# Optimization experiments

Hardware: AMD Instinct MI355X
Metric: run time of the kernel (lower is better)

Reference implementation:

```python
import jax, jax.numpy as jnp
import numpy as np

B, T, D = 2, 1024, 1024
NUM_HEADS_ARG = 16
HS = D // NUM_HEADS_ARG          # 64 (per-head size)
H = HS                           # bug in source: num_heads passed = head_size -> 64 heads
FF = 4 * D
EPS = 1e-5


def _layernorm(x, gamma, beta):
    mu = jnp.mean(x, axis=-1, keepdims=True)
    var = jnp.mean(jnp.square(x - mu), axis=-1, keepdims=True)
    return (x - mu) * jax.lax.rsqrt(var + EPS) * gamma + beta


def setup_inputs() -> dict:
    key = jax.random.key(0)
    ks = jax.random.split(key, 12)
    s_d = 1.0 / np.sqrt(D)
    s_cat = 1.0 / np.sqrt(H * HS)
    s_ff = 1.0 / np.sqrt(FF)
    return {
        "x": jax.random.normal(ks[0], (B, T, D), jnp.float32),
        "Wq": jax.random.uniform(ks[1], (H, D, HS), jnp.float32, -s_d, s_d),
        "Wk": jax.random.uniform(ks[2], (H, D, HS), jnp.float32, -s_d, s_d),
        "Wv": jax.random.uniform(ks[3], (H, D, HS), jnp.float32, -s_d, s_d),
        "Wo": jax.random.uniform(ks[4], (H * HS, D), jnp.float32, -s_cat, s_cat),
        "bo": jax.random.uniform(ks[5], (D,), jnp.float32, -s_cat, s_cat),
        "W1": jax.random.uniform(ks[6], (D, FF), jnp.float32, -s_d, s_d),
        "b1": jax.random.uniform(ks[7], (FF,), jnp.float32, -s_d, s_d),
        "W2": jax.random.uniform(ks[8], (FF, D), jnp.float32, -s_ff, s_ff),
        "b2": jax.random.uniform(ks[9], (D,), jnp.float32, -s_ff, s_ff),
        "g1": jnp.ones((D,), jnp.float32),
        "be1": jnp.zeros((D,), jnp.float32),
        "g2": jnp.ones((D,), jnp.float32),
        "be2": jnp.zeros((D,), jnp.float32),
    }


def reference(x, Wq, Wk, Wv, Wo, bo, W1, b1, W2, b2, g1, be1, g2, be2):
    # per-head projections (no bias): [B,H,T,hs]
    q = jnp.einsum('btd,hde->bhte', x, Wq)
    k = jnp.einsum('btd,hde->bhte', x, Wk)
    v = jnp.einsum('btd,hde->bhte', x, Wv)
    scores = jnp.einsum('bhte,bhse->bhts', q, k) / np.sqrt(HS)  # [B,H,T,T]
    causal = jnp.tril(jnp.ones((T, T), bool))
    scores = jnp.where(causal, scores, -jnp.inf)
    probs = jax.nn.softmax(scores, axis=-1)
    att = jnp.einsum('bhts,bhse->bhte', probs, v)               # [B,H,T,hs]
    # torch stack(dim=3) -> [B,T,hs,H] then flatten: index = d*H + h
    cat = jnp.transpose(att, (0, 2, 3, 1)).reshape(B, T, HS * H)
    mha = cat @ Wo + bo
    x1 = _layernorm(x + mha, g1, be1)
    ff = jax.nn.relu(x1 @ W1 + b1) @ W2 + b2
    return _layernorm(x1 + ff, g2, be2)
```

## Files before the change

### kernel.cpp

```cpp
#include <hip/hip_runtime.h>

typedef unsigned short u16;
typedef __bf16 bf16x8 __attribute__((ext_vector_type(8)));
typedef float f32x4 __attribute__((ext_vector_type(4)));

#define B_ 2
#define T_ 1024
#define D_ 1024
#define H_ 64
#define HS_ 64
#define FF_ 4096
#define SZ_QKV 8388608L
#define S_SCALE 0.1803368801111f

__device__ __forceinline__ float bf2f(u16 u) {
  union { unsigned int v; float f; } x; x.v = ((unsigned int)u) << 16; return x.f;
}
__device__ __forceinline__ u16 f2bf(float f) {
  union { float f; unsigned int v; } x; x.f = f;
  unsigned int r = x.v + 0x7fffu + ((x.v >> 16) & 1u);
  return (u16)(r >> 16);
}
__device__ __forceinline__ u16 f2bf_rtz(float f) {
  union { float f; unsigned int v; } x; x.f = f;
  return (u16)(x.v >> 16);
}

typedef __attribute__((address_space(3))) unsigned int lds_u32;
typedef __attribute__((address_space(1))) const unsigned int glb_u32;
__device__ __forceinline__ void gload_lds16(const void* g, void* l) {
  __builtin_amdgcn_global_load_lds((glb_u32*)g, (lds_u32*)l, 16, 0, 0);
}

__global__ __launch_bounds__(256) void prep(
    const float* __restrict__ x, const float* __restrict__ Wq,
    const float* __restrict__ Wk, const float* __restrict__ Wv,
    const float* __restrict__ Wo, const float* __restrict__ W1,
    const float* __restrict__ W2,
    u16* __restrict__ xb, u16* __restrict__ Wqkvt, u16* __restrict__ Wot,
    u16* __restrict__ W1t, u16* __restrict__ W2t)
{
  __shared__ float tile[64][65];
  int id = blockIdx.x;
  if (id < 1024) {
    const long i = ((long)id * 256 + threadIdx.x) * 8;
    float4 a = *(const float4*)(x + i);
    float4 b = *(const float4*)(x + i + 4);
    union { uint4 v; u16 u[8]; } o;
    o.u[0]=f2bf(a.x); o.u[1]=f2bf(a.y); o.u[2]=f2bf(a.z); o.u[3]=f2bf(a.w);
    o.u[4]=f2bf(b.x); o.u[5]=f2bf(b.y); o.u[6]=f2bf(b.z); o.u[7]=f2bf(b.w);
    *(uint4*)(xb + i) = o.v;
    return;
  }
  id -= 1024;
  const float* in; u16* out; long ibase, obase; int in_rs, out_rs, r0, c0;
  if (id < 3072) {
    const int w = id >> 10, rem = id & 1023;
    const int z = rem >> 4, rt = rem & 15;
    in = (w == 0) ? Wq : (w == 1) ? Wk : Wv;
    ibase = (long)z * 65536; in_rs = 64; r0 = rt * 64; c0 = 0;
    out = Wqkvt + (long)w * 4194304;
    obase = (long)z * 65536; out_rs = 1024;
  } else if (id < 4096) {
    const int rem = id - 3072;
    const int z = rem >> 4, ct = rem & 15;
    in = Wo; ibase = (long)z * 1024; in_rs = 65536; r0 = 0; c0 = ct * 64;
    out = Wot; obase = (long)z * 64; out_rs = 4096;
  } else if (id < 5120) {
    const int rem = id - 4096;
    const int rt = rem >> 6, ct = rem & 63;
    in = W1; ibase = 0; in_rs = 4096; r0 = rt * 64; c0 = ct * 64;
    out = W1t; obase = 0; out_rs = 1024;
  } else {
    const int rem = id - 5120;
    const int rt = rem >> 4, ct = rem & 15;
    in = W2; ibase = 0; in_rs = 1024; r0 = rt * 64; c0 = ct * 64;
    out = W2t; obase = 0; out_rs = 4096;
  }
  const int t = threadIdx.x, lr = t >> 4, lc4 = (t & 15) * 4;
  #pragma unroll
  for (int j = 0; j < 4; ++j) {
    float4 f = *(const float4*)(in + ibase + (long)(r0 + lr + j * 16) * in_rs + c0 + lc4);
    tile[lr + j * 16][lc4]     = f.x;
    tile[lr + j * 16][lc4 + 1] = f.y;
    tile[lr + j * 16][lc4 + 2] = f.z;
    tile[lr + j * 16][lc4 + 3] = f.w;
  }
  __syncthreads();
  const int cr = t >> 3, ch = t & 7;
  #pragma unroll
  for (int j2 = 0; j2 < 2; ++j2) {
    const int crr = cr + j2 * 32;
    union { uint4 v; u16 u[8]; } o;
    #pragma unroll
    for (int i = 0; i < 8; ++i) o.u[i] = f2bf(tile[ch * 8 + i][crr]);
    *(uint4*)(out + obase + (long)(c0 + crr) * out_rs + r0 + ch * 8) = o.v;
  }
}

template<int EPI, int LDA, int LDB>
__global__ __launch_bounds__(512, 2) void gemm8b(
    const u16* __restrict__ A, const u16* __restrict__ Bt, u16* __restrict__ C,
    const float* __restrict__ bias, int K, int koff, int ldc)
{
  __shared__ __attribute__((aligned(16))) u16 As[3][256 * 64];
  __shared__ __attribute__((aligned(16))) u16 Bs[3][128 * 64];
  const int nwg = gridDim.x, cpx = nwg >> 3;
  const int sid = (blockIdx.x & 7) * cpx + (blockIdx.x >> 3);
  const int bm = sid & 7, bn = sid >> 3;
  const int bz = blockIdx.z;
  const long ko = (long)bz * koff;
  const int tid = threadIdx.x, wave = tid >> 6, lane = tid & 63;
  const int quad = lane >> 4, l16 = lane & 15;
  const int wm = (wave >> 1) * 64;
  const int wn = (wave & 1) * 64;
  const int slog = ((tid & 7) ^ ((tid >> 3) & 7)) * 8;
  const int srow = tid >> 3;
  const int ph0 = ((quad)     ^ (l16 & 7)) * 8;
  const int ph1 = ((4 + quad) ^ (l16 & 7)) * 8;

  const u16* Ag = A + (long)(bm * 256) * LDA + ko + slog;
  const u16* Bg = Bt + (long)(bn * 128) * LDB + ko + slog;

  f32x4 acc[4][4];
  #pragma unroll
  for (int i = 0; i < 4; ++i)
    #pragma unroll
    for (int j = 0; j < 4; ++j) acc[i][j] = (f32x4){0.f, 0.f, 0.f, 0.f};

  const int nK = K >> 6;

  auto STAGE_A = [&](int d, int t, int a) {
    gload_lds16(Ag + (long)(a * 64 + srow) * LDA + (t << 6),
                (u16*)As[d] + a * 4096 + tid * 8);
  };
  auto STAGE_B = [&](int d, int t, int b) {
    gload_lds16(Bg + (long)(b * 64 + srow) * LDB + (t << 6),
                (u16*)Bs[d] + b * 4096 + tid * 8);
  };

  #pragma unroll
  for (int a = 0; a < 4; ++a) STAGE_A(0, 0, a);
  STAGE_B(0, 0, 0); STAGE_B(0, 0, 1);
  #pragma unroll
  for (int a = 0; a < 4; ++a) STAGE_A(1, 1, a);
  STAGE_B(1, 1, 0); STAGE_B(1, 1, 1);

  bf16x8 af[4][2], bf[4][2];
  int cur = 0;
  for (int t = 0; t < nK; ++t) {
    const int nxt = (cur >= 1) ? cur - 1 : 2;
    const bool st = (t + 2) < nK;
    const u16* Ab = As[cur];
    const u16* Bb = Bs[cur];

    if (t < nK - 1) { asm volatile("s_waitcnt vmcnt(6)" ::: "memory"); }
    else            { asm volatile("s_waitcnt vmcnt(0)" ::: "memory"); }
    __builtin_amdgcn_sched_barrier(0);
    __builtin_amdgcn_s_barrier();
    __builtin_amdgcn_sched_barrier(0);

    #pragma unroll
    for (int ii = 0; ii < 2; ++ii) {
      const u16* r = Ab + (wm + ii * 16 + l16) * 64;
      af[ii][0] = *(const bf16x8*)(r + ph0);
      af[ii][1] = *(const bf16x8*)(r + ph1);
    }
    #pragma unroll
    for (int jj = 0; jj < 2; ++jj) {
      const u16* r = Bb + (wn + jj * 16 + l16) * 64;
      bf[jj][0] = *(const bf16x8*)(r + ph0);
      bf[jj][1] = *(const bf16x8*)(r + ph1);
    }
    if (st) { STAGE_A(nxt, t + 2, 0); STAGE_A(nxt, t + 2, 1); }
    __builtin_amdgcn_sched_barrier(0);
    __builtin_amdgcn_s_setprio(1);
    #pragma unroll
    for (int ks = 0; ks < 2; ++ks)
      #pragma unroll
      for (int ii = 0; ii < 2; ++ii)
        #pragma unroll
        for (int jj = 0; jj < 2; ++jj)
          acc[ii][jj] = __builtin_amdgcn_mfma_f32_16x16x32_bf16(af[ii][ks], bf[jj][ks], acc[ii][jj], 0, 0, 0);
    __builtin_amdgcn_s_setprio(0);
    __builtin_amdgcn_sched_barrier(0);

    #pragma unroll
    for (int jj = 0; jj < 2; ++jj) {
      const u16* r = Bb + (wn + (2 + jj) * 16 + l16) * 64;
      bf[2 + jj][0] = *(const bf16x8*)(r + ph0);
      bf[2 + jj][1] = *(const bf16x8*)(r + ph1);
    }
    if (st) { STAGE_A(nxt, t + 2, 2); STAGE_A(nxt, t + 2, 3); }
    __builtin_amdgcn_sched_barrier(0);
    __builtin_amdgcn_s_setprio(1);
    #pragma unroll
    for (int ks = 0; ks < 2; ++ks)
      #pragma unroll
      for (int ii = 0; ii < 2; ++ii)
        #pragma unroll
        for (int jj = 0; jj < 2; ++jj)
          acc[ii][2 + jj] = __builtin_amdgcn_mfma_f32_16x16x32_bf16(af[ii][ks], bf[2 + jj][ks], acc[ii][2 + jj], 0, 0, 0);
    __builtin_amdgcn_s_setprio(0);
    __builtin_amdgcn_sched_barrier(0);

    #pragma unroll
    for (int ii = 0; ii < 2; ++ii) {
      const u16* r = Ab + (wm + (2 + ii) * 16 + l16) * 64;
      af[2 + ii][0] = *(const bf16x8*)(r + ph0);
      af[2 + ii][1] = *(const bf16x8*)(r + ph1);
    }
    if (st) { STAGE_B(nxt, t + 2, 0); STAGE_B(nxt, t + 2, 1); }
    __builtin_amdgcn_sched_barrier(0);
    __builtin_amdgcn_s_setprio(1);
    #pragma unroll
    for (int ks = 0; ks < 2; ++ks)
      #pragma unroll
      for (int ii = 0; ii < 2; ++ii)
        #pragma unroll
        for (int jj = 0; jj < 2; ++jj)
          acc[2 + ii][jj] = __builtin_amdgcn_mfma_f32_16x16x32_bf16(af[2 + ii][ks], bf[jj][ks], acc[2 + ii][jj], 0, 0, 0);
    __builtin_amdgcn_s_setprio(0);
    __builtin_amdgcn_sched_barrier(0);

    __builtin_amdgcn_s_setprio(1);
    #pragma unroll
    for (int ks = 0; ks < 2; ++ks)
      #pragma unroll
      for (int ii = 0; ii < 2; ++ii)
        #pragma unroll
        for (int jj = 0; jj < 2; ++jj)
          acc[2 + ii][2 + jj] = __builtin_amdgcn_mfma_f32_16x16x32_bf16(af[2 + ii][ks], bf[2 + jj][ks], acc[2 + ii][2 + jj], 0, 0, 0);
    __builtin_amdgcn_s_setprio(0);

    cur = (cur == 2) ? 0 : cur + 1;
  }

  float bv[4];
  #pragma unroll
  for (int j = 0; j < 4; ++j)
    bv[j] = (EPI == 1) ? bias[bn * 128 + wn + j * 16 + l16] : 0.f;
  #pragma unroll
  for (int i = 0; i < 4; ++i) {
    #pragma unroll
    for (int r = 0; r < 4; ++r) {
      const int row = bm * 256 + wm + i * 16 + quad * 4 + r;
      #pragma unroll
      for (int j = 0; j < 4; ++j) {
        const int col = bn * 128 + wn + j * 16 + l16;
        float vv = acc[i][j][r] + bv[j];
        if (EPI == 1) vv = fmaxf(vv, 0.f);
        if (EPI == 2) {
          const int which = col >> 12, rem = col & 4095;
          const int h = rem >> 6, e = rem & 63;
          const int bb = row >> 10, tt = row & 1023;
          C[(long)which * SZ_QKV + ((long)((bb << 6) + h)) * 65536L + tt * 64 + e] = f2bf(vv);
        } else if (EPI == 3) {
          ((float*)C)[(long)bz * 2097152 + (long)row * ldc + col] = vv;
        } else {
          C[(long)row * ldc + col] = f2bf(vv);
        }
      }
    }
  }
}

__global__ __launch_bounds__(256) void attn_flash(
    const u16* __restrict__ Q, const u16* __restrict__ Kg,
    const u16* __restrict__ V, u16* __restrict__ Om)
{
  __shared__ __attribute__((aligned(16))) u16 Ks[2][64][72];
  __shared__ __attribute__((aligned(16))) u16 Vs[2][64][72];
  __shared__ __attribute__((aligned(16))) u16 QP[4][16][72];
  const int bh = blockIdx.x;
  const int qt = gridDim.y - 1 - blockIdx.y;
  const int b = bh >> 6, h = bh & 63;
  const long base = (long)bh * (T_ * HS_);
  const int tid = threadIdx.x;
  const int wave = tid >> 6, lane = tid & 63, quad = lane >> 4, l16 = lane & 15;
  const int sm = tid >> 2, sc = (tid & 3) * 16;
  const int vswz = (sc >> 4) << 3;

  {
    const int qr = lane >> 3, qe = (lane & 7) * 8;
    #pragma unroll
    for (int j = 0; j < 2; ++j) {
      union { uint4 v; u16 u[8]; } a, o;
      a.v = *(const uint4*)(Q + base + (long)(qt * 64 + wave * 16 + qr + j * 8) * HS_ + qe);
      #pragma unroll
      for (int i = 0; i < 8; ++i) o.u[i] = f2bf(bf2f(a.u[i]) * S_SCALE);
      *(uint4*)&QP[wave][qr + j * 8][qe] = o.v;
    }
  }
  bf16x8 aq0 = *(const bf16x8*)&QP[wave][l16][quad * 8];
  bf16x8 aq1 = *(const bf16x8*)&QP[wave][l16][32 + quad * 8];

  float psum[4] = { 0.f, 0.f, 0.f, 0.f };
  f32x4 oacc[4] = { {0,0,0,0}, {0,0,0,0}, {0,0,0,0}, {0,0,0,0} };

  uint4 kA, kB, vA, vB;
  kA = *(const uint4*)(Kg + base + (long)sm * HS_ + sc);
  kB = *(const uint4*)(Kg + base + (long)sm * HS_ + sc + 8);
  vA = *(const uint4*)(V  + base + (long)sm * HS_ + sc);
  vB = *(const uint4*)(V  + base + (long)sm * HS_ + sc + 8);
  {
    *(uint4*)&Ks[0][sm][sc] = kA; *(uint4*)&Ks[0][sm][sc + 8] = kB;
    union { uint4 v; u16 u[8]; } t0, t1; t0.v = vA; t1.v = vB;
    #pragma unroll
    for (int i = 0; i < 8; ++i) Vs[0][sc + i][sm ^ vswz] = t0.u[i];
    #pragma unroll
    for (int i = 0; i < 8; ++i) Vs[0][sc + 8 + i][sm ^ vswz] = t1.u[i];
  }
  __syncthreads();

  for (int kt = 0; kt <= qt; ++kt) {
    const int cur = kt & 1;
    const bool pf = (kt < qt);
    if (pf) {
      const long nb = base + (long)((kt + 1) * 64 + sm) * HS_ + sc;
      kA = *(const uint4*)(Kg + nb); kB = *(const uint4*)(Kg + nb + 8);
      vA = *(const uint4*)(V  + nb); vB = *(const uint4*)(V  + nb + 8);
    }

    f32x4 sacc[4] = { {0,0,0,0}, {0,0,0,0}, {0,0,0,0}, {0,0,0,0} };
    #pragma unroll
    for (int nt = 0; nt < 4; ++nt) {
      bf16x8 b0 = *(const bf16x8*)&Ks[cur][nt * 16 + l16][quad * 8];
      bf16x8 b1 = *(const bf16x8*)&Ks[cur][nt * 16 + l16][32 + quad * 8];
      sacc[nt] = __builtin_amdgcn_mfma_f32_16x16x32_bf16(aq0, b0, sacc[nt], 0, 0, 0);
      sacc[nt] = __builtin_amdgcn_mfma_f32_16x16x32_bf16(aq1, b1, sacc[nt], 0, 0, 0);
    }

    if (kt == qt) {
      #pragma unroll
      for (int nt = 0; nt < 4; ++nt) {
        const int col = nt * 16 + l16;
        #pragma unroll
        for (int r = 0; r < 4; ++r) {
          const int row = wave * 16 + quad * 4 + r;
          float p = exp2f(sacc[nt][r]);
          p = (col <= row) ? p : 0.f;
          sacc[nt][r] = p; psum[r] += p;
        }
      }
    } else {
      #pragma unroll
      for (int nt = 0; nt < 4; ++nt)
        #pragma unroll
        for (int r = 0; r < 4; ++r) {
          const float p = exp2f(sacc[nt][r]);
          sacc[nt][r] = p; psum[r] += p;
        }
    }

    #pragma unroll
    for (int nt = 0; nt < 4; ++nt)
      #pragma unroll
      for (int r = 0; r < 4; ++r)
        QP[wave][quad * 4 + r][nt * 16 + l16] = f2bf_rtz(sacc[nt][r]);
    bf16x8 p0 = *(const bf16x8*)&QP[wave][l16][quad * 8];
    bf16x8 p1 = *(const bf16x8*)&QP[wave][l16][32 + quad * 8];

    #pragma unroll
    for (int et = 0; et < 4; ++et) {
      const int c0 = ((quad ^ et) * 8);
      bf16x8 b0 = *(const bf16x8*)&Vs[cur][et * 16 + l16][c0];
      bf16x8 b1 = *(const bf16x8*)&Vs[cur][et * 16 + l16][32 + c0];
      oacc[et] = __builtin_amdgcn_mfma_f32_16x16x32_bf16(p0, b0, oacc[et], 0, 0, 0);
      oacc[et] = __builtin_amdgcn_mfma_f32_16x16x32_bf16(p1, b1, oacc[et], 0, 0, 0);
    }

    if (pf) {
      const int nxt = 1 - cur;
      *(uint4*)&Ks[nxt][sm][sc] = kA; *(uint4*)&Ks[nxt][sm][sc + 8] = kB;
      union { uint4 v; u16 u[8]; } t0, t1; t0.v = vA; t1.v = vB;
      #pragma unroll
      for (int i = 0; i < 8; ++i) Vs[nxt][sc + i][sm ^ vswz] = t0.u[i];
      #pragma unroll
      for (int i = 0; i < 8; ++i) Vs[nxt][sc + 8 + i][sm ^ vswz] = t1.u[i];
    }
    __syncthreads();
  }

  #pragma unroll
  for (int off = 1; off < 16; off <<= 1)
    #pragma unroll
    for (int r = 0; r < 4; ++r)
      psum[r] += __shfl_xor(psum[r], off, 64);
  u16 (*Os)[72] = Ks[0];
  #pragma unroll
  for (int r = 0; r < 4; ++r) {
    const float rinv = 1.f / fmaxf(psum[r], 1e-20f);
    const int row = wave * 16 + quad * 4 + r;
    #pragma unroll
    for (int et = 0; et < 4; ++et)
      Os[row][et * 16 + l16] = f2bf(oacc[et][r] * rinv);
  }
  const int orow = wave * 16 + (lane >> 3), oe = (lane & 7) * 8;
  #pragma unroll
  for (int it = 0; it < 2; ++it) {
    const int rr = orow + it * 8;
    uint4 o = *(const uint4*)&Os[rr][oe];
    *(uint4*)(Om + ((long)(b * T_ + qt * 64 + rr)) * 4096 + h * 64 + oe) = o;
  }
}

template<int XBF, int OBF>
__global__ __launch_bounds__(256) void ln_sum4(
    const float* __restrict__ P4, const float* __restrict__ bias,
    const void* __restrict__ Xv, const float* __restrict__ g,
    const float* __restrict__ be, void* __restrict__ outv)
{
  __shared__ float red[8];
  const int row = blockIdx.x, tid = threadIdx.x;
  const long base = (long)row * D_;
  float v4[4]; float s = 0.f;
  #pragma unroll
  for (int j = 0; j < 4; ++j) {
    const int i = tid + j * 256;
    float acc = bias[i];
    #pragma unroll
    for (int p = 0; p < 4; ++p) acc += P4[(long)p * 2097152 + base + i];
    const float xval = XBF ? bf2f(((const u16*)Xv)[base + i]) : ((const float*)Xv)[base + i];
    v4[j] = xval + acc;
    s += v4[j];
  }
  #pragma unroll
  for (int off = 32; off > 0; off >>= 1) s += __shfl_down(s, off, 64);
  if ((tid & 63) == 0) red[tid >> 6] = s;
  __syncthreads();
  const float mu = (red[0] + red[1] + red[2] + red[3]) * (1.f / D_);
  float vs = 0.f;
  #pragma unroll
  for (int j = 0; j < 4; ++j) { const float d = v4[j] - mu; vs += d * d; }
  #pragma unroll
  for (int off = 32; off > 0; off >>= 1) vs += __shfl_down(vs, off, 64);
  __syncthreads();
  if ((tid & 63) == 0) red[tid >> 6] = vs;
  __syncthreads();
  const float rs = rsqrtf((red[0] + red[1] + red[2] + red[3]) * (1.f / D_) + 1e-5f);
  #pragma unroll
  for (int j = 0; j < 4; ++j) {
    const int i = tid + j * 256;
    const float o = (v4[j] - mu) * rs * g[i] + be[i];
    if (OBF) ((u16*)outv)[base + i] = f2bf(o);
    else     ((float*)outv)[base + i] = o;
  }
}

extern "C" void kernel_launch(void* const* d_in, const int* in_sizes, int n_in,
                              void* d_out, int out_size, void* d_ws, size_t ws_size,
                              hipStream_t stream) {
  const float* x   = (const float*)d_in[0];
  const float* Wq  = (const float*)d_in[1];
  const float* Wk  = (const float*)d_in[2];
  const float* Wv  = (const float*)d_in[3];
  const float* Wo  = (const float*)d_in[4];
  const float* bo  = (const float*)d_in[5];
  const float* W1  = (const float*)d_in[6];
  const float* b1  = (const float*)d_in[7];
  const float* W2  = (const float*)d_in[8];
  const float* b2  = (const float*)d_in[9];
  const float* g1  = (const float*)d_in[10];
  const float* be1 = (const float*)d_in[11];
  const float* g2  = (const float*)d_in[12];
  const float* be2 = (const float*)d_in[13];
  float* out = (float*)d_out;

  u16* ws = (u16*)d_ws;
  u16* xb    = ws;
  u16* Wqkvt = xb + 2097152;
  u16* Wot   = Wqkvt + 12582912;
  u16* W1t   = Wot + 4194304;
  u16* W2t   = W1t + 4194304;
  u16* q     = W2t + 4194304;
  u16* k     = q + SZ_QKV;
  u16* v     = k + SZ_QKV;
  u16* Om    = v + SZ_QKV;
  float* P1 = (float*)q;
  float* P2 = (float*)q;
  u16* x1  = v;
  u16* h1  = Om;

  dim3 blk(256);
  dim3 blk8(512);

  prep<<<dim3(7168), blk, 0, stream>>>(x, Wq, Wk, Wv, Wo, W1, W2,
                                       xb, Wqkvt, Wot, W1t, W2t);

  gemm8b<2, 1024, 1024><<<dim3(768), blk8, 0, stream>>>(
      xb, Wqkvt, q, nullptr, 1024, 0, 0);

  attn_flash<<<dim3(128, 16), blk, 0, stream>>>(q, k, v, Om);

  gemm8b<3, 4096, 4096><<<dim3(64, 1, 4), blk8, 0, stream>>>(
      Om, Wot, (u16*)P1, nullptr, 1024, 1024, 1024);

  ln_sum4<0, 1><<<dim3(2048), blk, 0, stream>>>(P1, bo, x, g1, be1, x1);

  gemm8b<1, 1024, 1024><<<dim3(256), blk8, 0, stream>>>(
      x1, W1t, h1, b1, 1024, 0, 4096);

  gemm8b<3, 4096, 4096><<<dim3(64, 1, 4), blk8, 0, stream>>>(
      h1, W2t, (u16*)P2, nullptr, 1024, 1024, 1024);

  ln_sum4<1, 0><<<dim3(2048), blk, 0, stream>>>(P2, b2, x1, g2, be2, out);

  (void)in_sizes; (void)n_in; (void)out_size; (void)ws_size;
}
```

Measured before the change: 358.8 us.

## Enlarge attention query tile to 128 rows with 8 waves per block

The flash attention kernel now processes 128 query rows per block using 512 threads (8 waves), so each staged K/V tile is shared by twice as many queries. This halves the grid in the query dimension and halves K/V global and LDS staging traffic per query row. Causal masking is generalized to global row/column indices for the last two key tiles, and output staging moves to the per-wave QP buffer. Waves covering the first 64 rows also compute a fully masked extra tile on the diagonal, and the larger blocks may reduce occupancy and causal load balance.

```diff
diff --git a/kernel.cpp b/kernel.cpp
--- a/kernel.cpp
+++ b/kernel.cpp
@@ -265,28 +265,29 @@
   }
 }
 
-__global__ __launch_bounds__(256) void attn_flash(
+__global__ __launch_bounds__(512) void attn_flash(
     const u16* __restrict__ Q, const u16* __restrict__ Kg,
     const u16* __restrict__ V, u16* __restrict__ Om)
 {
   __shared__ __attribute__((aligned(16))) u16 Ks[2][64][72];
   __shared__ __attribute__((aligned(16))) u16 Vs[2][64][72];
-  __shared__ __attribute__((aligned(16))) u16 QP[4][16][72];
+  __shared__ __attribute__((aligned(16))) u16 QP[8][16][72];
   const int bh = blockIdx.x;
-  const int qt = gridDim.y - 1 - blockIdx.y;
+  const int qb = gridDim.y - 1 - blockIdx.y;
   const int b = bh >> 6, h = bh & 63;
   const long base = (long)bh * (T_ * HS_);
   const int tid = threadIdx.x;
   const int wave = tid >> 6, lane = tid & 63, quad = lane >> 4, l16 = lane & 15;
-  const int sm = tid >> 2, sc = (tid & 3) * 16;
+  const int sm = tid >> 3, sc = (tid & 7) * 8;
   const int vswz = (sc >> 4) << 3;
+  const int qrow0 = qb * 128;
 
   {
     const int qr = lane >> 3, qe = (lane & 7) * 8;
     #pragma unroll
     for (int j = 0; j < 2; ++j) {
       union { uint4 v; u16 u[8]; } a, o;
-      a.v = *(const uint4*)(Q + base + (long)(qt * 64 + wave * 16 + qr + j * 8) * HS_ + qe);
+      a.v = *(const uint4*)(Q + base + (long)(qrow0 + wave * 16 + qr + j * 8) * HS_ + qe);
       #pragma unroll
       for (int i = 0; i < 8; ++i) o.u[i] = f2bf(bf2f(a.u[i]) * S_SCALE);
       *(uint4*)&QP[wave][qr + j * 8][qe] = o.v;
@@ -298,28 +299,25 @@
   float psum[4] = { 0.f, 0.f, 0.f, 0.f };
   f32x4 oacc[4] = { {0,0,0,0}, {0,0,0,0}, {0,0,0,0}, {0,0,0,0} };
 
-  uint4 kA, kB, vA, vB;
+  uint4 kA, vA;
   kA = *(const uint4*)(Kg + base + (long)sm * HS_ + sc);
-  kB = *(const uint4*)(Kg + base + (long)sm * HS_ + sc + 8);
   vA = *(const uint4*)(V  + base + (long)sm * HS_ + sc);
-  vB = *(const uint4*)(V  + base + (long)sm * HS_ + sc + 8);
   {
-    *(uint4*)&Ks[0][sm][sc] = kA; *(uint4*)&Ks[0][sm][sc + 8] = kB;
-    union { uint4 v; u16 u[8]; } t0, t1; t0.v = vA; t1.v = vB;
+    *(uint4*)&Ks[0][sm][sc] = kA;
+    union { uint4 v; u16 u[8]; } t0; t0.v = vA;
     #pragma unroll
     for (int i = 0; i < 8; ++i) Vs[0][sc + i][sm ^ vswz] = t0.u[i];
-    #pragma unroll
-    for (int i = 0; i < 8; ++i) Vs[0][sc + 8 + i][sm ^ vswz] = t1.u[i];
   }
   __syncthreads();
 
-  for (int kt = 0; kt <= qt; ++kt) {
+  const int ktmax = 2 * qb + 1;
+  for (int kt = 0; kt <= ktmax; ++kt) {
     const int cur = kt & 1;
-    const bool pf = (kt < qt);
+    const bool pf = (kt < ktmax);
     if (pf) {
       const long nb = base + (long)((kt + 1) * 64 + sm) * HS_ + sc;
-      kA = *(const uint4*)(Kg + nb); kB = *(const uint4*)(Kg + nb + 8);
-      vA = *(const uint4*)(V  + nb); vB = *(const uint4*)(V  + nb + 8);
+      kA = *(const uint4*)(Kg + nb);
+      vA = *(const uint4*)(V  + nb);
     }
 
     f32x4 sacc[4] = { {0,0,0,0}, {0,0,0,0}, {0,0,0,0}, {0,0,0,0} };
@@ -331,15 +329,15 @@
       sacc[nt] = __builtin_amdgcn_mfma_f32_16x16x32_bf16(aq1, b1, sacc[nt], 0, 0, 0);
     }
 
-    if (kt == qt) {
+    if (kt >= 2 * qb) {
       #pragma unroll
       for (int nt = 0; nt < 4; ++nt) {
-        const int col = nt * 16 + l16;
+        const int gcol = kt * 64 + nt * 16 + l16;
         #pragma unroll
         for (int r = 0; r < 4; ++r) {
-          const int row = wave * 16 + quad * 4 + r;
+          const int grow = qrow0 + wave * 16 + quad * 4 + r;
           float p = exp2f(sacc[nt][r]);
-          p = (col <= row) ? p : 0.f;
+          p = (gcol <= grow) ? p : 0.f;
           sacc[nt][r] = p; psum[r] += p;
         }
       }
@@ -372,12 +370,10 @@
 
     if (pf) {
       const int nxt = 1 - cur;
-      *(uint4*)&Ks[nxt][sm][sc] = kA; *(uint4*)&Ks[nxt][sm][sc + 8] = kB;
-      union { uint4 v; u16 u[8]; } t0, t1; t0.v = vA; t1.v = vB;
+      *(uint4*)&Ks[nxt][sm][sc] = kA;
+      union { uint4 v; u16 u[8]; } t0; t0.v = vA;
       #pragma unroll
       for (int i = 0; i < 8; ++i) Vs[nxt][sc + i][sm ^ vswz] = t0.u[i];
-      #pragma unroll
-      for (int i = 0; i < 8; ++i) Vs[nxt][sc + 8 + i][sm ^ vswz] = t1.u[i];
     }
     __syncthreads();
   }
@@ -387,21 +383,21 @@
     #pragma unroll
     for (int r = 0; r < 4; ++r)
       psum[r] += __shfl_xor(psum[r], off, 64);
-  u16 (*Os)[72] = Ks[0];
+  u16 (*Os)[72] = QP[wave];
   #pragma unroll
   for (int r = 0; r < 4; ++r) {
     const float rinv = 1.f / fmaxf(psum[r], 1e-20f);
-    const int row = wave * 16 + quad * 4 + r;
+    const int rowl = quad * 4 + r;
     #pragma unroll
     for (int et = 0; et < 4; ++et)
-      Os[row][et * 16 + l16] = f2bf(oacc[et][r] * rinv);
-  }
-  const int orow = wave * 16 + (lane >> 3), oe = (lane & 7) * 8;
+      Os[rowl][et * 16 + l16] = f2bf(oacc[et][r] * rinv);
+  }
+  const int orow = lane >> 3, oe = (lane & 7) * 8;
   #pragma unroll
   for (int it = 0; it < 2; ++it) {
     const int rr = orow + it * 8;
     uint4 o = *(const uint4*)&Os[rr][oe];
-    *(uint4*)(Om + ((long)(b * T_ + qt * 64 + rr)) * 4096 + h * 64 + oe) = o;
+    *(uint4*)(Om + ((long)(b * T_ + qrow0 + wave * 16 + rr)) * 4096 + h * 64 + oe) = o;
   }
 }
 
@@ -491,7 +487,7 @@
   gemm8b<2, 1024, 1024><<<dim3(768), blk8, 0, stream>>>(
       xb, Wqkvt, q, nullptr, 1024, 0, 0);
 
-  attn_flash<<<dim3(128, 16), blk, 0, stream>>>(q, k, v, Om);
+  attn_flash<<<dim3(128, 8), blk8, 0, stream>>>(q, k, v, Om);
 
   gemm8b<3, 4096, 4096><<<dim3(64, 1, 4), blk8, 0, stream>>>(
       Om, Wot, (u16*)P1, nullptr, 1024, 1024, 1024);
```

New measurement: 367.7 us. +2.5%, slower.
